# Optimization experiments

Hardware: AMD Instinct MI355X
Metric: run time of the kernel (lower is better)

The kernel has to match this reference:

```python
import jax, jax.numpy as jnp
import numpy as np

B, S, D, H = 2, 2048, 1024, 16
HD = D // H  # 64

def _make_freqs():
    # flux-style rotation matrices: [1,1,S,HD//2,2,2]
    theta = 10000.0
    inv = 1.0 / (theta ** (np.arange(0, HD, 2, dtype=np.float32) / HD))  # [HD//2]
    pos = np.arange(S, dtype=np.float32)
    ang = pos[:, None] * inv[None, :]  # [S, HD//2]
    cos, sin = np.cos(ang), np.sin(ang)
    rot = np.stack([np.stack([cos, -sin], -1), np.stack([sin, cos], -1)], -2)  # [S,HD//2,2,2]
    return jnp.asarray(rot[None, None], dtype=jnp.float32)

def setup_inputs() -> dict:
    key = jax.random.key(0)
    ks = jax.random.split(key, 9)
    sc = 1.0 / np.sqrt(D)
    return {
        "x": jax.random.normal(ks[0], (B, S, D), jnp.float32),
        "freqs": _make_freqs(),
        "Wq": jax.random.normal(ks[1], (D, D), jnp.float32) * sc,
        "bq": jax.random.normal(ks[2], (D,), jnp.float32) * 0.01,
        "Wk": jax.random.normal(ks[3], (D, D), jnp.float32) * sc,
        "bk": jax.random.normal(ks[4], (D,), jnp.float32) * 0.01,
        "Wv": jax.random.normal(ks[5], (D, D), jnp.float32) * sc,
        "bv": jax.random.normal(ks[6], (D,), jnp.float32) * 0.01,
        "Wo": jax.random.normal(ks[7], (D, D), jnp.float32) * sc,
        "bo": jax.random.normal(ks[8], (D,), jnp.float32) * 0.01,
    }

def _apply_rope(xq, xk, freqs):
    # xq/xk: [B,H,S,HD]; freqs: [1,1,S,HD//2,2,2]
    def rot(t):
        t_ = t.reshape(*t.shape[:-1], -1, 1, 2)  # [B,H,S,HD//2,1,2]
        out = freqs[..., 0] * t_[..., 0] + freqs[..., 1] * t_[..., 1]  # [B,H,S,HD//2,2]
        return out.reshape(t.shape).astype(t.dtype)
    return rot(xq), rot(xk)

def reference(x, freqs, Wq, bq, Wk, bk, Wv, bv, Wo, bo):
    b, s, _ = x.shape
    # QKV projections (torch Linear: x @ W.T + b)
    q = (x @ Wq.T + bq).reshape(b, s, H, HD).transpose(0, 2, 1, 3)  # [B,H,S,HD]
    k = (x @ Wk.T + bk).reshape(b, s, H, HD).transpose(0, 2, 1, 3)
    v = (x @ Wv.T + bv).reshape(b, s, H, HD).transpose(0, 2, 1, 3)
    q, k = _apply_rope(q, k, freqs)
    # scaled dot product attention, no mask, no dropout
    scale = 1.0 / jnp.sqrt(jnp.asarray(HD, x.dtype))
    scores = jnp.einsum("bhqd,bhkd->bhqk", q, k) * scale
    attn = jax.nn.softmax(scores, axis=-1)
    o = jnp.einsum("bhqk,bhkd->bhqd", attn, v)  # [B,H,S,HD]
    o = o.transpose(0, 2, 1, 3).reshape(b, s, D)
    return o @ Wo.T + bo
```

## Files before the change

kernel.cpp:

```cpp
#include <hip/hip_runtime.h>
#include <cmath>

#define B_ 2
#define S_ 2048
#define D_ 1024
#define H_ 16
#define HD_ 64
#define M_ 4096

typedef __attribute__((ext_vector_type(8))) short short8;
typedef __attribute__((ext_vector_type(4))) short short4v;
typedef __attribute__((ext_vector_type(4))) float f32x4;

__device__ __forceinline__ short f2bf(float x) {
    unsigned u = __builtin_bit_cast(unsigned, x);
    u += 0x7fffu + ((u >> 16) & 1u);
    return (short)(u >> 16);
}

__device__ __forceinline__ void gload_lds16(const short* g, short* l) {
    __builtin_amdgcn_global_load_lds(
        (const __attribute__((address_space(1))) unsigned int*)g,
        (__attribute__((address_space(3))) unsigned int*)l, 16, 0, 0);
}

template<int N> __device__ __forceinline__ void vwait() {
    if constexpr (N == 0) asm volatile("s_waitcnt vmcnt(0)" ::: "memory");
    else if constexpr (N == 2) asm volatile("s_waitcnt vmcnt(2)" ::: "memory");
    else if constexpr (N == 3) asm volatile("s_waitcnt vmcnt(3)" ::: "memory");
    else if constexpr (N == 4) asm volatile("s_waitcnt vmcnt(4)" ::: "memory");
}
__device__ __forceinline__ void bar() { __builtin_amdgcn_s_barrier(); }

__global__ __launch_bounds__(256) void cast_all_kernel(
    const float* __restrict__ x,  const float* __restrict__ Wq,
    const float* __restrict__ Wk, const float* __restrict__ Wv,
    const float* __restrict__ Wo,
    short* __restrict__ xb, short* __restrict__ Wqkvb, short* __restrict__ Wob)
{
    const size_t i = (size_t)blockIdx.x * 256 + threadIdx.x;
    const float* src; short* dst; size_t off;
    if (i < 1048576)      { src = x;  dst = xb;              off = i; }
    else if (i < 1310720) { src = Wq; dst = Wqkvb;           off = i - 1048576; }
    else if (i < 1572864) { src = Wk; dst = Wqkvb + 1048576; off = i - 1310720; }
    else if (i < 1835008) { src = Wv; dst = Wqkvb + 2097152; off = i - 1572864; }
    else                  { src = Wo; dst = Wob;             off = i - 1835008; }
    float4 v = ((const float4*)src)[off];
    short4v o = { f2bf(v.x), f2bf(v.y), f2bf(v.z), f2bf(v.w) };
    ((short4v*)dst)[off] = o;
}

__global__ __launch_bounds__(256) void gemm_qkv(
    const short* __restrict__ A, const short* __restrict__ Bw,
    const float* __restrict__ b0p, const float* __restrict__ b1p, const float* __restrict__ b2p,
    const float* __restrict__ freqs,
    short* __restrict__ out0, short* __restrict__ out1, short* __restrict__ out2)
{
    constexpr int TM = 128, TN = 128, RT = 4, CT = 4, LPC = 4;
    __shared__ __align__(16) short A0[TM*32];
    __shared__ __align__(16) short A1[TM*32];
    __shared__ __align__(16) short A2[TM*32];
    __shared__ __align__(16) short B0[TN*32];
    __shared__ __align__(16) short B1[TN*32];
    __shared__ __align__(16) short B2[TN*32];
    const int t = threadIdx.x;
    const int w = t >> 6;
    const int lane = t & 63;
    const int qd = lane >> 4, l = lane & 15;
    const int bid = blockIdx.x;
    const int xcd = bid & 7, idx = bid >> 3;
    const int mr = (xcd & 3) * 8 + idx / 12;
    const int nc = (xcd >> 2) * 12 + idx % 12;
    const int n0 = nc * TN, m0 = mr * TM;
    const int wr = (w >> 1) * (TM/2), wc = (w & 1) * (TN/2);
    const int srow  = lane >> 2;
    const int sslot = ((lane & 3) ^ ((lane >> 3) & 3)) * 8;
    const int rsw = (l >> 1) & 3;

    f32x4 acc[RT][CT] = {};

    auto STAGE = [&](int c, short* As, short* Bss) {
        const int k0 = c * 32;
        #pragma unroll
        for (int j = 0; j < TM/64; ++j) {
            const int r0 = (j*4 + w) * 16;
            gload_lds16(A + (size_t)(m0 + r0 + srow)*1024 + k0 + sslot, &As[r0*32]);
        }
        #pragma unroll
        for (int j = 0; j < TN/64; ++j) {
            const int r0 = (j*4 + w) * 16;
            gload_lds16(Bw + (size_t)(n0 + r0 + srow)*1024 + k0 + sslot, &Bss[r0*32]);
        }
    };

    auto COMP = [&](const short* As, const short* Bss) {
        short8 af[RT], bfr[CT];
        #pragma unroll
        for (int rt = 0; rt < RT; ++rt)
            af[rt] = *(const short8*)&As[(wr + rt*16 + l)*32 + ((qd ^ rsw) << 3)];
        #pragma unroll
        for (int ct = 0; ct < CT; ++ct)
            bfr[ct] = *(const short8*)&Bss[(wc + ct*16 + l)*32 + ((qd ^ rsw) << 3)];
        #pragma unroll
        for (int rt = 0; rt < RT; ++rt)
            #pragma unroll
            for (int ct = 0; ct < CT; ++ct)
                acc[rt][ct] = __builtin_amdgcn_mfma_f32_16x16x32_bf16(af[rt], bfr[ct], acc[rt][ct], 0, 0, 0);
    };

    STAGE(0, A0, B0);
    STAGE(1, A1, B1);
    for (int p = 0; p <= 27; p += 3) {
        vwait<LPC>(); bar();
        STAGE(p + 2, A2, B2);
        COMP(A0, B0);
        vwait<LPC>(); bar();
        STAGE(p + 3, A0, B0);
        COMP(A1, B1);
        vwait<LPC>(); bar();
        STAGE(p + 4, A1, B1);
        COMP(A2, B2);
    }
    vwait<LPC>(); bar();
    COMP(A0, B0);
    vwait<0>(); bar();
    COMP(A1, B1);

    const int sel = n0 >> 10;
    const int nb = n0 & 1023;
    const float* bias = (sel == 0) ? b0p : (sel == 1) ? b1p : b2p;
    if (sel < 2) {
        short* outg = (sel == 0) ? out0 : out1;
        #pragma unroll
        for (int rt = 0; rt < RT; ++rt)
            #pragma unroll
            for (int ct = 0; ct < CT; ++ct) {
                const int d = nb + wc + ct*16 + l;
                const float bsv = bias[d];
                const int h = d >> 6, hd = d & 63;
                #pragma unroll
                for (int r = 0; r < 4; ++r) {
                    const int m = m0 + wr + rt*16 + qd*4 + r;
                    const int bb = m >> 11, s = m & 2047;
                    float val = acc[rt][ct][r] + bsv;
                    float pv = __shfl_xor(val, 1);
                    const float* f = freqs + (size_t)s*128 + (size_t)(hd >> 1)*4;
                    float o = (d & 1) ? (f[2]*pv + f[3]*val) : (f[0]*val + f[1]*pv);
                    outg[((size_t)(bb*16 + h)*2048 + s)*64 + hd] = f2bf(o);
                }
            }
    } else {
        #pragma unroll
        for (int rt = 0; rt < RT; ++rt)
            #pragma unroll
            for (int ct = 0; ct < CT; ++ct) {
                const int d = nb + wc + ct*16 + l;
                const float bsv = bias[d];
                const int h = d >> 6, hd = d & 63;
                const int m0r = m0 + wr + rt*16 + qd*4;
                const int bb = m0r >> 11, s0 = m0r & 2047;
                short4v pk;
                #pragma unroll
                for (int r = 0; r < 4; ++r) pk[r] = f2bf(acc[rt][ct][r] + bsv);
                *(short4v*)&out2[((size_t)(bb*16 + h)*64 + hd)*2048 + s0] = pk;
            }
    }
}

__global__ __launch_bounds__(256) void gemm_proj64(
    const short* __restrict__ A, const short* __restrict__ Bw,
    const float* __restrict__ b0p, float* __restrict__ out)
{
    __shared__ __align__(16) short A0[64*64];
    __shared__ __align__(16) short A1[64*64];
    __shared__ __align__(16) short A2[64*64];
    __shared__ __align__(16) short B0[64*64];
    __shared__ __align__(16) short B1[64*64];
    __shared__ __align__(16) short B2[64*64];
    const int t = threadIdx.x;
    const int w = t >> 6;
    const int lane = t & 63;
    const int qd = lane >> 4, l = lane & 15;
    const int l7 = lane & 7;
    const int bid = blockIdx.x;
    const int xcd = bid & 7, idx = bid >> 3;
    const int mr = xcd * 8 + (idx >> 4);
    const int nc = idx & 15;
    const int n0 = nc * 64, m0 = mr * 64;
    const int wr = (w >> 1) * 32, wc = (w & 1) * 32;
    const int rl  = lane >> 3;
    const int ss8 = ((lane & 7) ^ rl) << 3;

    f32x4 acc[2][2] = {};

    auto STAGE = [&](int c, short* As, short* Bss) {
        const int k0 = c * 64;
        #pragma unroll
        for (int j = 0; j < 2; ++j) {
            const int r0 = (j*4 + w) * 8;
            gload_lds16(A  + (size_t)(m0 + r0 + rl)*1024 + k0 + ss8, &As[r0*64]);
            gload_lds16(Bw + (size_t)(n0 + r0 + rl)*1024 + k0 + ss8, &Bss[r0*64]);
        }
    };

    auto COMP = [&](const short* As, const short* Bss) {
        #pragma unroll
        for (int kk = 0; kk < 2; ++kk) {
            short8 af[2], bfr[2];
            #pragma unroll
            for (int rt = 0; rt < 2; ++rt)
                af[rt] = *(const short8*)&As[(wr + rt*16 + l)*64 + (((kk*4 + qd) ^ l7) << 3)];
            #pragma unroll
            for (int ct = 0; ct < 2; ++ct)
                bfr[ct] = *(const short8*)&Bss[(wc + ct*16 + l)*64 + (((kk*4 + qd) ^ l7) << 3)];
            #pragma unroll
            for (int rt = 0; rt < 2; ++rt)
                #pragma unroll
                for (int ct = 0; ct < 2; ++ct)
                    acc[rt][ct] = __builtin_amdgcn_mfma_f32_16x16x32_bf16(af[rt], bfr[ct], acc[rt][ct], 0, 0, 0);
        }
    };

    STAGE(0, A0, B0);
    STAGE(1, A1, B1);
    for (int p = 0; p <= 9; p += 3) {
        vwait<4>(); bar();
        STAGE(p + 2, A2, B2);
        COMP(A0, B0);
        vwait<4>(); bar();
        STAGE(p + 3, A0, B0);
        COMP(A1, B1);
        vwait<4>(); bar();
        STAGE(p + 4, A1, B1);
        COMP(A2, B2);
    }
    vwait<4>(); bar();
    STAGE(14, A2, B2);
    COMP(A0, B0);
    vwait<4>(); bar();
    STAGE(15, A0, B0);
    COMP(A1, B1);
    vwait<4>(); bar();
    COMP(A2, B2);
    vwait<0>(); bar();
    COMP(A0, B0);

    #pragma unroll
    for (int rt = 0; rt < 2; ++rt)
        #pragma unroll
        for (int ct = 0; ct < 2; ++ct) {
            const int n = n0 + wc + ct*16 + l;
            const float bias = b0p[n];
            #pragma unroll
            for (int r = 0; r < 4; ++r) {
                const int m = m0 + wr + rt*16 + qd*4 + r;
                out[(size_t)m*1024 + n] = acc[rt][ct][r] + bias;
            }
        }
}

__global__ __launch_bounds__(512) void attn_mfma(
    const short* __restrict__ qg, const short* __restrict__ kg,
    const short* __restrict__ vtg, short* __restrict__ og)
{
    __shared__ __align__(16) short K0[64*64];
    __shared__ __align__(16) short K1[64*64];
    __shared__ __align__(16) short K2[64*64];
    __shared__ __align__(16) short V0[64*64];
    __shared__ __align__(16) short V1[64*64];
    __shared__ __align__(16) short V2[64*64];
    __shared__ __align__(16) short Pb[128*64];

    const int t = threadIdx.x;
    const int w = t >> 6;
    const int lane = t & 63;
    const int qd = lane >> 4, l = lane & 15;
    const int l7 = lane & 7;
    const int bid = blockIdx.x;
    const int xcd = bid & 7, idx = bid >> 3;
    const int bh = xcd * 4 + (idx >> 4);
    const int q0 = (idx & 15) * 128;

    const int rl  = lane >> 3;
    const int ss8 = ((lane & 7) ^ rl) << 3;

    short8 qf[2];
    const short* qb = qg + ((size_t)bh*2048 + q0 + w*16)*64;
    #pragma unroll
    for (int kf = 0; kf < 2; ++kf)
        qf[kf] = *(const short8*)&qb[l*64 + kf*32 + qd*8];

    f32x4 oacc[4] = {};
    float lsum = 0.f;

    const short* kbase = kg  + (size_t)bh*2048*64;
    const short* vbase = vtg + (size_t)bh*64*2048;
    const float SC = 0.125f * 1.44269504088896340736f;

    auto PREF = [&](int c, short* Kd, short* Vd) {
        gload_lds16(kbase + (size_t)(c*64 + w*8 + rl)*64 + ss8,   &Kd[(w*8)*64]);
        gload_lds16(vbase + (size_t)(w*8 + rl)*2048 + c*64 + ss8, &Vd[(w*8)*64]);
    };

    auto TILE = [&](const short* Kc, const short* Vc) {
        f32x4 sacc[4] = {};
        #pragma unroll
        for (int ct = 0; ct < 4; ++ct) {
            short8 k0f = *(const short8*)&Kc[(ct*16 + l)*64 + (((0 + qd) ^ l7) << 3)];
            short8 k1f = *(const short8*)&Kc[(ct*16 + l)*64 + (((4 + qd) ^ l7) << 3)];
            sacc[ct] = __builtin_amdgcn_mfma_f32_16x16x32_bf16(k0f, qf[0], sacc[ct], 0, 0, 0);
            sacc[ct] = __builtin_amdgcn_mfma_f32_16x16x32_bf16(k1f, qf[1], sacc[ct], 0, 0, 0);
        }
        #pragma unroll
        for (int ct = 0; ct < 4; ++ct) {
            float p0 = exp2f(sacc[ct][0] * SC);
            float p1 = exp2f(sacc[ct][1] * SC);
            float p2 = exp2f(sacc[ct][2] * SC);
            float p3 = exp2f(sacc[ct][3] * SC);
            lsum += (p0 + p1) + (p2 + p3);
            union { unsigned u[2]; short4v s; } cv;
            asm("v_cvt_pk_bf16_f32 %0, %1, %2" : "=v"(cv.u[0]) : "v"(p0), "v"(p1));
            asm("v_cvt_pk_bf16_f32 %0, %1, %2" : "=v"(cv.u[1]) : "v"(p2), "v"(p3));
            *(short4v*)&Pb[(w*16 + l)*64 + (((ct*32 + qd*8) ^ (l7 << 4)) >> 1)] = cv.s;
        }
        #pragma unroll
        for (int kf = 0; kf < 2; ++kf) {
            const int so = ((kf*4 + qd) ^ l7) << 3;
            short8 pa = *(const short8*)&Pb[(w*16 + l)*64 + so];
            #pragma unroll
            for (int ht = 0; ht < 4; ++ht) {
                short8 vb = *(const short8*)&Vc[(ht*16 + l)*64 + so];
                oacc[ht] = __builtin_amdgcn_mfma_f32_16x16x32_bf16(pa, vb, oacc[ht], 0, 0, 0);
            }
        }
    };

    PREF(0, K0, V0);
    PREF(1, K1, V1);
    for (int p = 0; p <= 27; p += 3) {
        vwait<2>(); bar();
        PREF(p + 2, K2, V2);
        TILE(K0, V0);
        vwait<2>(); bar();
        PREF(p + 3, K0, V0);
        TILE(K1, V1);
        vwait<2>(); bar();
        PREF(p + 4, K1, V1);
        TILE(K2, V2);
    }
    vwait<2>(); bar();
    TILE(K0, V0);
    vwait<0>(); bar();
    TILE(K1, V1);

    lsum += __shfl_xor(lsum, 16);
    lsum += __shfl_xor(lsum, 32);
    float inv[4];
    #pragma unroll
    for (int r = 0; r < 4; ++r)
        inv[r] = 1.0f / __shfl(lsum, qd*4 + r);

    const int bb = bh >> 4, h = bh & 15;
    #pragma unroll
    for (int ht = 0; ht < 4; ++ht)
        #pragma unroll
        for (int r = 0; r < 4; ++r) {
            const int s = q0 + w*16 + qd*4 + r;
            og[((size_t)bb*2048 + s)*1024 + h*64 + ht*16 + l] =
                f2bf(oacc[ht][r] * inv[r]);
        }
}

extern "C" void kernel_launch(void* const* d_in, const int* in_sizes, int n_in,
                              void* d_out, int out_size, void* d_ws, size_t ws_size,
                              hipStream_t stream)
{
    const float* x  = (const float*)d_in[0];
    const float* fr = (const float*)d_in[1];
    const float* Wq = (const float*)d_in[2];
    const float* bq = (const float*)d_in[3];
    const float* Wk = (const float*)d_in[4];
    const float* bk = (const float*)d_in[5];
    const float* Wv = (const float*)d_in[6];
    const float* bv = (const float*)d_in[7];
    const float* Wo = (const float*)d_in[8];
    const float* bo = (const float*)d_in[9];
    float* out = (float*)d_out;

    short* ws    = (short*)d_ws;
    short* xb    = ws;
    short* Wqkvb = xb    + 4194304;
    short* Wob   = Wqkvb + 3145728;
    short* qg    = Wob   + 1048576;
    short* kg    = qg    + 4194304;
    short* vtg   = kg    + 4194304;
    short* og    = vtg   + 4194304;

    cast_all_kernel<<<8192, 256, 0, stream>>>(x, Wq, Wk, Wv, Wo, xb, Wqkvb, Wob);
    gemm_qkv<<<768, 256, 0, stream>>>(xb, Wqkvb, bq, bk, bv, fr, qg, kg, vtg);
    attn_mfma<<<512, 512, 0, stream>>>(qg, kg, vtg, og);
    gemm_proj64<<<1024, 256, 0, stream>>>(og, Wob, bo, out);
}
```

Before: 239.4 us.

## Enlarge QKV GEMM tiles to 256x256 with 512 threads and double buffering

Measured after the change: 241.4 us. No clear change (+0.8%).

```diff
diff --git a/kernel.cpp b/kernel.cpp
--- a/kernel.cpp
+++ b/kernel.cpp
@@ -27,7 +27,6 @@
 template<int N> __device__ __forceinline__ void vwait() {
     if constexpr (N == 0) asm volatile("s_waitcnt vmcnt(0)" ::: "memory");
     else if constexpr (N == 2) asm volatile("s_waitcnt vmcnt(2)" ::: "memory");
-    else if constexpr (N == 3) asm volatile("s_waitcnt vmcnt(3)" ::: "memory");
     else if constexpr (N == 4) asm volatile("s_waitcnt vmcnt(4)" ::: "memory");
 }
 __device__ __forceinline__ void bar() { __builtin_amdgcn_s_barrier(); }
@@ -50,81 +49,76 @@
     ((short4v*)dst)[off] = o;
 }
 
-__global__ __launch_bounds__(256) void gemm_qkv(
+__global__ __launch_bounds__(512, 2) void gemm_qkv256(
     const short* __restrict__ A, const short* __restrict__ Bw,
     const float* __restrict__ b0p, const float* __restrict__ b1p, const float* __restrict__ b2p,
     const float* __restrict__ freqs,
     short* __restrict__ out0, short* __restrict__ out1, short* __restrict__ out2)
 {
-    constexpr int TM = 128, TN = 128, RT = 4, CT = 4, LPC = 4;
-    __shared__ __align__(16) short A0[TM*32];
-    __shared__ __align__(16) short A1[TM*32];
-    __shared__ __align__(16) short A2[TM*32];
-    __shared__ __align__(16) short B0[TN*32];
-    __shared__ __align__(16) short B1[TN*32];
-    __shared__ __align__(16) short B2[TN*32];
+    __shared__ __align__(16) short A0[256*64];
+    __shared__ __align__(16) short A1[256*64];
+    __shared__ __align__(16) short B0[256*64];
+    __shared__ __align__(16) short B1[256*64];
     const int t = threadIdx.x;
     const int w = t >> 6;
     const int lane = t & 63;
     const int qd = lane >> 4, l = lane & 15;
+    const int l7 = lane & 7;
     const int bid = blockIdx.x;
     const int xcd = bid & 7, idx = bid >> 3;
-    const int mr = (xcd & 3) * 8 + idx / 12;
-    const int nc = (xcd >> 2) * 12 + idx % 12;
-    const int n0 = nc * TN, m0 = mr * TM;
-    const int wr = (w >> 1) * (TM/2), wc = (w & 1) * (TN/2);
-    const int srow  = lane >> 2;
-    const int sslot = ((lane & 3) ^ ((lane >> 3) & 3)) * 8;
-    const int rsw = (l >> 1) & 3;
-
-    f32x4 acc[RT][CT] = {};
+    const int mr = xcd * 2 + idx / 12;
+    const int nc = idx % 12;
+    const int m0 = mr * 256, n0 = nc * 256;
+    const int wr = (w >> 2) * 128;
+    const int wc = (w & 3) * 64;
+    const int rl  = lane >> 3;
+    const int ss8 = ((lane & 7) ^ rl) << 3;
+
+    f32x4 acc[8][4] = {};
 
     auto STAGE = [&](int c, short* As, short* Bss) {
-        const int k0 = c * 32;
-        #pragma unroll
-        for (int j = 0; j < TM/64; ++j) {
-            const int r0 = (j*4 + w) * 16;
-            gload_lds16(A + (size_t)(m0 + r0 + srow)*1024 + k0 + sslot, &As[r0*32]);
-        }
-        #pragma unroll
-        for (int j = 0; j < TN/64; ++j) {
-            const int r0 = (j*4 + w) * 16;
-            gload_lds16(Bw + (size_t)(n0 + r0 + srow)*1024 + k0 + sslot, &Bss[r0*32]);
+        const int k0 = c * 64;
+        #pragma unroll
+        for (int j = 0; j < 4; ++j) {
+            const int r0 = j*64 + w*8;
+            gload_lds16(A + (size_t)(m0 + r0 + rl)*1024 + k0 + ss8, &As[r0*64]);
+        }
+        #pragma unroll
+        for (int j = 0; j < 4; ++j) {
+            const int r0 = j*64 + w*8;
+            gload_lds16(Bw + (size_t)(n0 + r0 + rl)*1024 + k0 + ss8, &Bss[r0*64]);
         }
     };
 
     auto COMP = [&](const short* As, const short* Bss) {
-        short8 af[RT], bfr[CT];
-        #pragma unroll
-        for (int rt = 0; rt < RT; ++rt)
-            af[rt] = *(const short8*)&As[(wr + rt*16 + l)*32 + ((qd ^ rsw) << 3)];
-        #pragma unroll
-        for (int ct = 0; ct < CT; ++ct)
-            bfr[ct] = *(const short8*)&Bss[(wc + ct*16 + l)*32 + ((qd ^ rsw) << 3)];
-        #pragma unroll
-        for (int rt = 0; rt < RT; ++rt)
-            #pragma unroll
-            for (int ct = 0; ct < CT; ++ct)
-                acc[rt][ct] = __builtin_amdgcn_mfma_f32_16x16x32_bf16(af[rt], bfr[ct], acc[rt][ct], 0, 0, 0);
+        #pragma unroll
+        for (int kk = 0; kk < 2; ++kk) {
+            short8 af[8], bfr[4];
+            #pragma unroll
+            for (int rt = 0; rt < 8; ++rt)
+                af[rt] = *(const short8*)&As[(wr + rt*16 + l)*64 + (((kk*4 + qd) ^ l7) << 3)];
+            #pragma unroll
+            for (int ct = 0; ct < 4; ++ct)
+                bfr[ct] = *(const short8*)&Bss[(wc + ct*16 + l)*64 + (((kk*4 + qd) ^ l7) << 3)];
+            #pragma unroll
+            for (int rt = 0; rt < 8; ++rt)
+                #pragma unroll
+                for (int ct = 0; ct < 4; ++ct)
+                    acc[rt][ct] = __builtin_amdgcn_mfma_f32_16x16x32_bf16(af[rt], bfr[ct], acc[rt][ct], 0, 0, 0);
+        }
     };
 
     STAGE(0, A0, B0);
-    STAGE(1, A1, B1);
-    for (int p = 0; p <= 27; p += 3) {
-        vwait<LPC>(); bar();
-        STAGE(p + 2, A2, B2);
+    vwait<0>(); bar();
+    for (int p = 0; p < 16; p += 2) {
+        STAGE(p + 1, A1, B1);
         COMP(A0, B0);
-        vwait<LPC>(); bar();
-        STAGE(p + 3, A0, B0);
+        vwait<0>(); bar();
+        if (p + 2 < 16)
+            STAGE(p + 2, A0, B0);
         COMP(A1, B1);
-        vwait<LPC>(); bar();
-        STAGE(p + 4, A1, B1);
-        COMP(A2, B2);
+        vwait<0>(); bar();
     }
-    vwait<LPC>(); bar();
-    COMP(A0, B0);
-    vwait<0>(); bar();
-    COMP(A1, B1);
 
     const int sel = n0 >> 10;
     const int nb = n0 & 1023;
@@ -132,9 +126,9 @@
     if (sel < 2) {
         short* outg = (sel == 0) ? out0 : out1;
         #pragma unroll
-        for (int rt = 0; rt < RT; ++rt)
-            #pragma unroll
-            for (int ct = 0; ct < CT; ++ct) {
+        for (int rt = 0; rt < 8; ++rt)
+            #pragma unroll
+            for (int ct = 0; ct < 4; ++ct) {
                 const int d = nb + wc + ct*16 + l;
                 const float bsv = bias[d];
                 const int h = d >> 6, hd = d & 63;
@@ -151,9 +145,9 @@
             }
     } else {
         #pragma unroll
-        for (int rt = 0; rt < RT; ++rt)
-            #pragma unroll
-            for (int ct = 0; ct < CT; ++ct) {
+        for (int rt = 0; rt < 8; ++rt)
+            #pragma unroll
+            for (int ct = 0; ct < 4; ++ct) {
                 const int d = nb + wc + ct*16 + l;
                 const float bsv = bias[d];
                 const int h = d >> 6, hd = d & 63;
@@ -397,7 +391,7 @@
     short* og    = vtg   + 4194304;
 
     cast_all_kernel<<<8192, 256, 0, stream>>>(x, Wq, Wk, Wv, Wo, xb, Wqkvb, Wob);
-    gemm_qkv<<<768, 256, 0, stream>>>(xb, Wqkvb, bq, bk, bv, fr, qg, kg, vtg);
+    gemm_qkv256<<<192, 512, 0, stream>>>(xb, Wqkvb, bq, bk, bv, fr, qg, kg, vtg);
     attn_mfma<<<512, 512, 0, stream>>>(qg, kg, vtg, og);
     gemm_proj64<<<1024, 256, 0, stream>>>(og, Wob, bo, out);
 }
```

## Make output projection GEMM wave-private to drop block barriers

Applied to the files above, without the earlier changes.

Result: slower. 248.4 us (+3.8%).

```diff
diff --git a/kernel.cpp b/kernel.cpp
--- a/kernel.cpp
+++ b/kernel.cpp
@@ -27,7 +27,6 @@
 template<int N> __device__ __forceinline__ void vwait() {
     if constexpr (N == 0) asm volatile("s_waitcnt vmcnt(0)" ::: "memory");
     else if constexpr (N == 2) asm volatile("s_waitcnt vmcnt(2)" ::: "memory");
-    else if constexpr (N == 3) asm volatile("s_waitcnt vmcnt(3)" ::: "memory");
     else if constexpr (N == 4) asm volatile("s_waitcnt vmcnt(4)" ::: "memory");
 }
 __device__ __forceinline__ void bar() { __builtin_amdgcn_s_barrier(); }
@@ -167,93 +166,76 @@
     }
 }
 
-__global__ __launch_bounds__(256) void gemm_proj64(
+__global__ __launch_bounds__(256) void gemm_proj_wf(
     const short* __restrict__ A, const short* __restrict__ Bw,
     const float* __restrict__ b0p, float* __restrict__ out)
 {
-    __shared__ __align__(16) short A0[64*64];
-    __shared__ __align__(16) short A1[64*64];
-    __shared__ __align__(16) short A2[64*64];
-    __shared__ __align__(16) short B0[64*64];
-    __shared__ __align__(16) short B1[64*64];
-    __shared__ __align__(16) short B2[64*64];
+    __shared__ __align__(16) short A0[4][32*32];
+    __shared__ __align__(16) short A1[4][32*32];
+    __shared__ __align__(16) short B0[4][32*32];
+    __shared__ __align__(16) short B1[4][32*32];
     const int t = threadIdx.x;
     const int w = t >> 6;
     const int lane = t & 63;
     const int qd = lane >> 4, l = lane & 15;
-    const int l7 = lane & 7;
     const int bid = blockIdx.x;
     const int xcd = bid & 7, idx = bid >> 3;
-    const int mr = xcd * 8 + (idx >> 4);
-    const int nc = idx & 15;
-    const int n0 = nc * 64, m0 = mr * 64;
-    const int wr = (w >> 1) * 32, wc = (w & 1) * 32;
-    const int rl  = lane >> 3;
-    const int ss8 = ((lane & 7) ^ rl) << 3;
+    const int mrB = xcd * 8 + (idx >> 4);
+    const int ncB = idx & 15;
+    const int m0 = mrB * 64 + (w >> 1) * 32;
+    const int n0 = ncB * 64 + (w & 1) * 32;
+    const int srow  = lane >> 2;
+    const int sslot = ((lane & 3) ^ ((lane >> 3) & 3)) * 8;
+    const int rsw = (l >> 1) & 3;
+
+    short* a0 = &A0[w][0]; short* a1 = &A1[w][0];
+    short* b0 = &B0[w][0]; short* b1 = &B1[w][0];
 
     f32x4 acc[2][2] = {};
 
-    auto STAGE = [&](int c, short* As, short* Bss) {
-        const int k0 = c * 64;
-        #pragma unroll
-        for (int j = 0; j < 2; ++j) {
-            const int r0 = (j*4 + w) * 8;
-            gload_lds16(A  + (size_t)(m0 + r0 + rl)*1024 + k0 + ss8, &As[r0*64]);
-            gload_lds16(Bw + (size_t)(n0 + r0 + rl)*1024 + k0 + ss8, &Bss[r0*64]);
-        }
-    };
-
-    auto COMP = [&](const short* As, const short* Bss) {
-        #pragma unroll
-        for (int kk = 0; kk < 2; ++kk) {
-            short8 af[2], bfr[2];
-            #pragma unroll
-            for (int rt = 0; rt < 2; ++rt)
-                af[rt] = *(const short8*)&As[(wr + rt*16 + l)*64 + (((kk*4 + qd) ^ l7) << 3)];
+    auto STAGE = [&](int c, short* As, short* Bs) {
+        const int k0 = c * 32;
+        gload_lds16(A  + (size_t)(m0 + srow)*1024 + k0 + sslot,      &As[0]);
+        gload_lds16(A  + (size_t)(m0 + 16 + srow)*1024 + k0 + sslot, &As[16*32]);
+        gload_lds16(Bw + (size_t)(n0 + srow)*1024 + k0 + sslot,      &Bs[0]);
+        gload_lds16(Bw + (size_t)(n0 + 16 + srow)*1024 + k0 + sslot, &Bs[16*32]);
+    };
+
+    auto COMP = [&](const short* As, const short* Bs) {
+        short8 af[2], bfr[2];
+        #pragma unroll
+        for (int rt = 0; rt < 2; ++rt)
+            af[rt] = *(const short8*)&As[(rt*16 + l)*32 + ((qd ^ rsw) << 3)];
+        #pragma unroll
+        for (int ct = 0; ct < 2; ++ct)
+            bfr[ct] = *(const short8*)&Bs[(ct*16 + l)*32 + ((qd ^ rsw) << 3)];
+        #pragma unroll
+        for (int rt = 0; rt < 2; ++rt)
             #pragma unroll
             for (int ct = 0; ct < 2; ++ct)
-                bfr[ct] = *(const short8*)&Bss[(wc + ct*16 + l)*64 + (((kk*4 + qd) ^ l7) << 3)];
-            #pragma unroll
-            for (int rt = 0; rt < 2; ++rt)
-                #pragma unroll
-                for (int ct = 0; ct < 2; ++ct)
-                    acc[rt][ct] = __builtin_amdgcn_mfma_f32_16x16x32_bf16(af[rt], bfr[ct], acc[rt][ct], 0, 0, 0);
-        }
-    };
-
-    STAGE(0, A0, B0);
-    STAGE(1, A1, B1);
-    for (int p = 0; p <= 9; p += 3) {
-        vwait<4>(); bar();
-        STAGE(p + 2, A2, B2);
-        COMP(A0, B0);
-        vwait<4>(); bar();
-        STAGE(p + 3, A0, B0);
-        COMP(A1, B1);
-        vwait<4>(); bar();
-        STAGE(p + 4, A1, B1);
-        COMP(A2, B2);
+                acc[rt][ct] = __builtin_amdgcn_mfma_f32_16x16x32_bf16(af[rt], bfr[ct], acc[rt][ct], 0, 0, 0);
+    };
+
+    STAGE(0, a0, b0);
+    for (int p = 0; p < 30; p += 2) {
+        STAGE(p + 1, a1, b1);
+        vwait<4>(); COMP(a0, b0);
+        STAGE(p + 2, a0, b0);
+        vwait<4>(); COMP(a1, b1);
     }
-    vwait<4>(); bar();
-    STAGE(14, A2, B2);
-    COMP(A0, B0);
-    vwait<4>(); bar();
-    STAGE(15, A0, B0);
-    COMP(A1, B1);
-    vwait<4>(); bar();
-    COMP(A2, B2);
-    vwait<0>(); bar();
-    COMP(A0, B0);
+    STAGE(31, a1, b1);
+    vwait<4>(); COMP(a0, b0);
+    vwait<0>(); COMP(a1, b1);
 
     #pragma unroll
     for (int rt = 0; rt < 2; ++rt)
         #pragma unroll
         for (int ct = 0; ct < 2; ++ct) {
-            const int n = n0 + wc + ct*16 + l;
+            const int n = n0 + ct*16 + l;
             const float bias = b0p[n];
             #pragma unroll
             for (int r = 0; r < 4; ++r) {
-                const int m = m0 + wr + rt*16 + qd*4 + r;
+                const int m = m0 + rt*16 + qd*4 + r;
                 out[(size_t)m*1024 + n] = acc[rt][ct][r] + bias;
             }
         }
@@ -399,5 +381,5 @@
     cast_all_kernel<<<8192, 256, 0, stream>>>(x, Wq, Wk, Wv, Wo, xb, Wqkvb, Wob);
     gemm_qkv<<<768, 256, 0, stream>>>(xb, Wqkvb, bq, bk, bv, fr, qg, kg, vtg);
     attn_mfma<<<512, 512, 0, stream>>>(qg, kg, vtg, og);
-    gemm_proj64<<<1024, 256, 0, stream>>>(og, Wob, bo, out);
-}
+    gemm_proj_wf<<<1024, 256, 0, stream>>>(og, Wob, bo, out);
+}
```
